# Performance work log

Hardware: AMD Instinct MI355X
Metric: run time of the kernel (lower is better)

Reference implementation:

```python
import jax, jax.numpy as jnp
import numpy as np
from jax import lax

EPS = 1e-5
DN = ('NCHW', 'OIHW', 'NCHW')


def fastsign(x):
    # forward: sign(x); (STE backward handled in fwdbwd module)
    return jnp.sign(x)


def batchnorm(x, gamma, beta, mean, var):
    # inference-mode BatchNorm2d over channel dim
    inv = gamma / jnp.sqrt(var + EPS)
    return x * inv[None, :, None, None] + (beta - mean * inv)[None, :, None, None]


def avgpool2x2(x):
    B, C, H, W = x.shape
    return x.reshape(B, C, H // 2, 2, W // 2, 2).mean(axis=(3, 5))


def setup_inputs() -> dict:
    key = jax.random.key(0)
    ks = jax.random.split(key, 8)
    inp, B, H, W = 256, 32, 56, 56
    x = jax.random.normal(ks[0], (B, inp, H, W), dtype=jnp.float32)
    w3 = jax.random.normal(ks[1], (inp, inp, 3, 3), dtype=jnp.float32) * 0.05
    g3 = jax.random.uniform(ks[2], (inp,), dtype=jnp.float32, minval=0.5, maxval=1.5)
    b3 = jax.random.normal(ks[3], (inp,), dtype=jnp.float32) * 0.1
    m3 = jax.random.normal(ks[4], (inp,), dtype=jnp.float32) * 0.1
    v3 = jax.random.uniform(ks[5], (inp,), dtype=jnp.float32, minval=0.5, maxval=1.5)
    w1 = jax.random.normal(ks[6], (2 * inp, inp, 1, 1), dtype=jnp.float32) * 0.05
    k2 = jax.random.split(ks[7], 4)
    g1 = jax.random.uniform(k2[0], (2 * inp,), dtype=jnp.float32, minval=0.5, maxval=1.5)
    b1 = jax.random.normal(k2[1], (2 * inp,), dtype=jnp.float32) * 0.1
    m1 = jax.random.normal(k2[2], (2 * inp,), dtype=jnp.float32) * 0.1
    v1 = jax.random.uniform(k2[3], (2 * inp,), dtype=jnp.float32, minval=0.5, maxval=1.5)
    return {"x": x, "w3": w3, "g3": g3, "b3": b3, "m3": m3, "v3": v3,
            "w1": w1, "g1": g1, "b1": b1, "m1": m1, "v1": v1}


def reference(x, w3, g3, b3, m3, v3, w1, g1, b1, m1, v1):
    stride = 2
    # --- conv3x3 branch: binarize act + binarize weight, stride-2 3x3 conv, BN ---
    y = lax.conv_general_dilated(fastsign(x), fastsign(w3),
                                 window_strides=(stride, stride),
                                 padding=((1, 1), (1, 1)),
                                 dimension_numbers=DN)
    y = batchnorm(y, g3, b3, m3, v3)
    # shortcut1: AvgPool2d(2,2) when stride==2
    h = y + avgpool2x2(x)
    # --- pointwise branch: 1x1 binary conv doubling channels, BN ---
    z = lax.conv_general_dilated(fastsign(h), fastsign(w1),
                                 window_strides=(1, 1),
                                 padding=((0, 0), (0, 0)),
                                 dimension_numbers=DN)
    z = batchnorm(z, g1, b1, m1, v1)
    # shortcut2: duplicate channels
    return z + jnp.concatenate((h, h), axis=1)
```

## Files before the change

kernel.cpp:

```cpp
#include <hip/hip_runtime.h>
#include <stdint.h>

#define BB   32
#define CC1  256
#define HH   56
#define WW   56
#define PH   57
#define OHH  28
#define OWW  28
#define NPIX (OHH*OWW)
#define CC2  512
#define EPSV 1e-5f

typedef unsigned short ushortx8 __attribute__((ext_vector_type(8)));

static __device__ __forceinline__ int popc64(uint64_t v) {
    return __builtin_popcountll(v);
}
static __device__ __forceinline__ unsigned short f2bf(float f) {
    uint32_t u = __float_as_uint(f);
    u += 0x7FFFu + ((u >> 16) & 1u);
    return (unsigned short)(u >> 16);
}
static __device__ __forceinline__ float bf2f(unsigned short u) {
    return __uint_as_float(((uint32_t)u) << 16);
}

__global__ __launch_bounds__(256) void k_binpool(const float* __restrict__ x,
                                                 uint64_t* __restrict__ xbp,
                                                 uint64_t* __restrict__ hbits,
                                                 unsigned short* __restrict__ pool) {
    int gid = blockIdx.x * 256 + threadIdx.x;
    hbits[gid] = 0ull;
    if (gid < 7296) {
        int b = gid / 228, r = gid % 228;
        xbp[((size_t)(b * PH) * PH + (r >> 2)) * 4 + (r & 3)] = 0ull;
    } else if (gid < 14464) {
        int i = gid - 7296;
        int b = i / 224, r = i % 224;
        xbp[((size_t)(b * PH + (r >> 2) + 1) * PH) * 4 + (r & 3)] = 0ull;
    }

    int cell = gid % NPIX;
    int cg   = (gid / NPIX) & 3;
    int b    = gid / (NPIX * 4);
    int pw = cell % OWW;
    int ph = cell / OWW;
    int h0 = 2 * ph, w0 = 2 * pw;
    const float* base = x + ((size_t)(b * CC1 + cg * 64)) * (HH * WW) + h0 * WW + w0;

    uint64_t s00 = 0, s01 = 0, s10 = 0, s11 = 0;
    for (int j = 0; j < 8; ++j) {
        ushortx8 pv;
        #pragma unroll
        for (int i = 0; i < 8; ++i) {
            int c = j * 8 + i;
            const float* cp = base + (size_t)c * (HH * WW);
            float2 a = *(const float2*)(cp);
            float2 d = *(const float2*)(cp + WW);
            s00 |= (uint64_t)(a.x >= 0.0f) << c;
            s01 |= (uint64_t)(a.y >= 0.0f) << c;
            s10 |= (uint64_t)(d.x >= 0.0f) << c;
            s11 |= (uint64_t)(d.y >= 0.0f) << c;
            pv[i] = f2bf(0.25f * (a.x + a.y + d.x + d.y));
        }
        *(ushortx8*)(pool + ((size_t)((b * 32 + cg * 8 + j) * NPIX + cell)) * 8) = pv;
    }

    size_t rb = ((size_t)(b * PH + h0 + 1) * PH + w0 + 1) * 4 + cg;
    xbp[rb]          = s00;
    xbp[rb + 4]      = s01;
    xbp[rb + PH * 4]     = s10;
    xbp[rb + PH * 4 + 4] = s11;
}

__global__ __launch_bounds__(256) void k_packw3(const float* __restrict__ w3,
                                                uint64_t* __restrict__ w3t) {
    int id = blockIdx.x * 256 + threadIdx.x;
    int k   = id % 4;
    int tap = (id / 4) % 9;
    int oc  = id / 36;
    const float* wp = w3 + (size_t)oc * 2304 + (size_t)(k * 64) * 9 + tap;
    uint64_t bits = 0;
    #pragma unroll 8
    for (int c = 0; c < 64; ++c) {
        bits |= (uint64_t)(wp[c * 9] >= 0.0f) << c;
    }
    w3t[((size_t)tap * CC1 + oc) * 4 + k] = bits;
}

__global__ __launch_bounds__(256) void k_prep2(const float* __restrict__ w1,
                                               uint64_t* __restrict__ w1b,
                                               const uint64_t* __restrict__ w3t,
                                               const float* __restrict__ g3,
                                               const float* __restrict__ b3,
                                               const float* __restrict__ m3,
                                               const float* __restrict__ v3,
                                               const float* __restrict__ g1,
                                               const float* __restrict__ b1,
                                               const float* __restrict__ m1,
                                               const float* __restrict__ v1,
                                               float* __restrict__ sc3,
                                               float* __restrict__ bi3,
                                               float* __restrict__ sc1,
                                               float* __restrict__ bi1,
                                               int* __restrict__ ctop,
                                               int* __restrict__ cleft,
                                               int* __restrict__ ccorn) {
    int id = blockIdx.x * 256 + threadIdx.x;
    int k  = id % 4;
    int oc = id / 4;
    const float* wp = w1 + (size_t)oc * 256 + k * 64;
    uint64_t bits = 0;
    #pragma unroll 8
    for (int c = 0; c < 64; ++c) {
        bits |= (uint64_t)(wp[c] >= 0.0f) << c;
    }
    w1b[(size_t)oc * 4 + k] = bits;
    if (k == 0) {
        float s1 = g1[oc] / sqrtf(v1[oc] + EPSV);
        sc1[oc] = s1;
        bi1[oc] = b1[oc] - m1[oc] * s1;
        if (oc < CC1) {
            float s3 = g3[oc] / sqrtf(v3[oc] + EPSV);
            sc3[oc] = s3;
            bi3[oc] = b3[oc] - m3[oc] * s3;
        }
    }
    if (id < CC1) {
        int pt[9];
        #pragma unroll
        for (int t = 0; t < 9; ++t) {
            const uint64_t* p = w3t + ((size_t)t * CC1 + id) * 4;
            pt[t] = popc64(p[0]) + popc64(p[1]) + popc64(p[2]) + popc64(p[3]);
        }
        ctop[id]  = (256 - 2 * pt[0]) + (256 - 2 * pt[1]) + (256 - 2 * pt[2]);
        cleft[id] = (256 - 2 * pt[0]) + (256 - 2 * pt[3]) + (256 - 2 * pt[6]);
        ccorn[id] = (256 - 2 * pt[0]);
    }
}

__global__ __launch_bounds__(256, 4) void k_conv3(const uint64_t* __restrict__ xbp,
                                                  const uint64_t* __restrict__ w3t,
                                                  const float* __restrict__ sc3,
                                                  const float* __restrict__ bi3,
                                                  const int* __restrict__ ctop,
                                                  const int* __restrict__ cleft,
                                                  const int* __restrict__ ccorn,
                                                  const unsigned short* __restrict__ pool,
                                                  unsigned short* __restrict__ hbuf,
                                                  uint64_t* __restrict__ hbits) {
    int loc = blockIdx.x * 256 + threadIdx.x;
    int p  = loc % NPIX;
    int ow = p % OWW;
    int oh = p / OWW;
    int b  = loc / NPIX;
    int ocg = blockIdx.y;

    int tot[8] = {0, 0, 0, 0, 0, 0, 0, 0};
    for (int kh = 0; kh < 3; ++kh) {
        const uint64_t* rp = xbp + ((size_t)((b * PH + 2 * oh + kh) * PH) + 2 * ow) * 4;
        uint64_t t0[4], t1[4], t2[4];
        #pragma unroll
        for (int k = 0; k < 4; ++k) { t0[k] = rp[k]; t1[k] = rp[4 + k]; t2[k] = rp[8 + k]; }
        const uint64_t* wrow = w3t + ((size_t)(kh * 3) * CC1 + ocg * 8) * 4;
        #pragma unroll
        for (int o = 0; o < 8; ++o) {
            const uint64_t* w0  = wrow + (size_t)o * 4;
            const uint64_t* w1p = w0 + (size_t)CC1 * 4;
            const uint64_t* w2p = w0 + (size_t)CC1 * 8;
            int s = tot[o];
            #pragma unroll
            for (int k = 0; k < 4; ++k) s += popc64(t0[k] ^ w0[k]);
            #pragma unroll
            for (int k = 0; k < 4; ++k) s += popc64(t1[k] ^ w1p[k]);
            #pragma unroll
            for (int k = 0; k < 4; ++k) s += popc64(t2[k] ^ w2p[k]);
            tot[o] = s;
        }
    }

    ushortx8 pv = *(const ushortx8*)(pool + ((size_t)((b * 32 + ocg) * NPIX + p)) * 8);

    bool top  = (oh == 0);
    bool left = (ow == 0);
    uint64_t hb = 0;
    #pragma unroll
    for (int o = 0; o < 8; ++o) {
        int oc = ocg * 8 + o;
        int corr = (top ? ctop[oc] : 0) + (left ? cleft[oc] : 0)
                 - ((top && left) ? ccorn[oc] : 0);
        float y = (float)(2304 - 2 * tot[o] - corr);
        float hv = y * sc3[oc] + bi3[oc] + bf2f(pv[o]);
        hbuf[((size_t)(b * CC1 + oc)) * NPIX + p] = f2bf(hv);
        hb |= (uint64_t)(hv >= 0.0f) << ((ocg & 7) * 8 + o);
    }
    atomicOr((unsigned long long*)&hbits[(size_t)loc * 4 + (ocg >> 3)],
             (unsigned long long)hb);
}

__global__ __launch_bounds__(256, 4) void k_conv1(const uint64_t* __restrict__ hbits,
                                                  const uint64_t* __restrict__ w1b,
                                                  const unsigned short* __restrict__ hbuf,
                                                  const float* __restrict__ sc1,
                                                  const float* __restrict__ bi1,
                                                  float* __restrict__ out) {
    int loc = blockIdx.x * 256 + threadIdx.x;
    int p = loc % NPIX;
    int b = loc / NPIX;
    int ocg = blockIdx.y;

    uint64_t hw[4];
    const uint64_t* hp = hbits + (size_t)loc * 4;
    #pragma unroll
    for (int k = 0; k < 4; ++k) hw[k] = hp[k];

    #pragma unroll
    for (int o = 0; o < 8; ++o) {
        int oc  = ocg * 8 + o;
        int oc2 = oc + CC1;
        const uint64_t* wa = w1b + (size_t)oc  * 4;
        const uint64_t* wb = w1b + (size_t)oc2 * 4;
        int pa = 0, pb = 0;
        #pragma unroll
        for (int k = 0; k < 4; ++k) pa += popc64(hw[k] ^ wa[k]);
        #pragma unroll
        for (int k = 0; k < 4; ++k) pb += popc64(hw[k] ^ wb[k]);
        float hc = bf2f(hbuf[((size_t)(b * CC1 + oc)) * NPIX + p]);
        float za = (float)(256 - 2 * pa) * sc1[oc]  + bi1[oc]  + hc;
        float zb = (float)(256 - 2 * pb) * sc1[oc2] + bi1[oc2] + hc;
        out[((size_t)(b * CC2 + oc))  * NPIX + p] = za;
        out[((size_t)(b * CC2 + oc2)) * NPIX + p] = zb;
    }
}

extern "C" void kernel_launch(void* const* d_in, const int* in_sizes, int n_in,
                              void* d_out, int out_size, void* d_ws, size_t ws_size,
                              hipStream_t stream) {
    const float* x  = (const float*)d_in[0];
    const float* w3 = (const float*)d_in[1];
    const float* g3 = (const float*)d_in[2];
    const float* b3 = (const float*)d_in[3];
    const float* m3 = (const float*)d_in[4];
    const float* v3 = (const float*)d_in[5];
    const float* w1 = (const float*)d_in[6];
    const float* g1 = (const float*)d_in[7];
    const float* b1 = (const float*)d_in[8];
    const float* m1 = (const float*)d_in[9];
    const float* v1 = (const float*)d_in[10];
    float* out = (float*)d_out;

    uint8_t* ws = (uint8_t*)d_ws;
    size_t off = 0;
    uint64_t* xbp   = (uint64_t*)(ws + off); off += (size_t)BB * PH * PH * 4 * 8;
    uint64_t* hbits = (uint64_t*)(ws + off); off += (size_t)BB * NPIX * 4 * 8;
    uint64_t* w3t   = (uint64_t*)(ws + off); off += (size_t)9 * CC1 * 4 * 8;
    uint64_t* w1b   = (uint64_t*)(ws + off); off += (size_t)CC2 * 4 * 8;
    float* sc3 = (float*)(ws + off); off += CC1 * 4;
    float* bi3 = (float*)(ws + off); off += CC1 * 4;
    float* sc1 = (float*)(ws + off); off += CC2 * 4;
    float* bi1 = (float*)(ws + off); off += CC2 * 4;
    int* ctop  = (int*)(ws + off); off += CC1 * 4;
    int* cleft = (int*)(ws + off); off += CC1 * 4;
    int* ccorn = (int*)(ws + off); off += CC1 * 4;
    unsigned short* pool   = (unsigned short*)(ws + off); off += (size_t)BB * CC1 * NPIX * 2;
    unsigned short* hbuf16 = (unsigned short*)(ws + off); off += (size_t)BB * CC1 * NPIX * 2;

    k_binpool<<<dim3(100352 / 256), 256, 0, stream>>>(x, xbp, hbits, pool);
    k_packw3 <<<dim3(9216 / 256),   256, 0, stream>>>(w3, w3t);
    k_prep2  <<<dim3(2048 / 256),   256, 0, stream>>>(w1, w1b, w3t, g3, b3, m3, v3,
                                                      g1, b1, m1, v1, sc3, bi3, sc1, bi1,
                                                      ctop, cleft, ccorn);
    k_conv3  <<<dim3(98, 32), 256, 0, stream>>>(xbp, w3t, sc3, bi3, ctop, cleft, ccorn,
                                                pool, hbuf16, hbits);
    k_conv1  <<<dim3(98, 32), 256, 0, stream>>>(hbits, w1b, hbuf16, sc1, bi1, out);
}
```

Baseline: 90.09 us.

## Fuse binary 3x3 conv and pointwise conv into one kernel via shared sign bits

Merges the stride-2 binary 3x3 conv kernel and the 1x1 binary conv kernel into a single kernel. Each block handles 16 pixels across all 256 channels, with 16 thread groups of 16 channels each, and exchanges the sign bits of h through shared memory. This removes the bf16 h buffer round trip, the hbits zeroing and the atomicOr. The 3x3 weights are relaid out per output channel, so each thread reads 12 contiguous words per kernel row. The cost is more registers per thread (16 accumulators plus 16 h values) and fewer threads per block working on distinct pixels, which may hurt coalescing of the output stores.

```diff
diff --git a/kernel.cpp b/kernel.cpp
--- a/kernel.cpp
+++ b/kernel.cpp
@@ -28,10 +28,8 @@
 
 __global__ __launch_bounds__(256) void k_binpool(const float* __restrict__ x,
                                                  uint64_t* __restrict__ xbp,
-                                                 uint64_t* __restrict__ hbits,
                                                  unsigned short* __restrict__ pool) {
     int gid = blockIdx.x * 256 + threadIdx.x;
-    hbits[gid] = 0ull;
     if (gid < 7296) {
         int b = gid / 228, r = gid % 228;
         xbp[((size_t)(b * PH) * PH + (r >> 2)) * 4 + (r & 3)] = 0ull;
@@ -68,14 +66,14 @@
     }
 
     size_t rb = ((size_t)(b * PH + h0 + 1) * PH + w0 + 1) * 4 + cg;
-    xbp[rb]          = s00;
-    xbp[rb + 4]      = s01;
+    xbp[rb]              = s00;
+    xbp[rb + 4]          = s01;
     xbp[rb + PH * 4]     = s10;
     xbp[rb + PH * 4 + 4] = s11;
 }
 
 __global__ __launch_bounds__(256) void k_packw3(const float* __restrict__ w3,
-                                                uint64_t* __restrict__ w3t) {
+                                                uint64_t* __restrict__ w3o) {
     int id = blockIdx.x * 256 + threadIdx.x;
     int k   = id % 4;
     int tap = (id / 4) % 9;
@@ -86,12 +84,12 @@
     for (int c = 0; c < 64; ++c) {
         bits |= (uint64_t)(wp[c * 9] >= 0.0f) << c;
     }
-    w3t[((size_t)tap * CC1 + oc) * 4 + k] = bits;
+    w3o[(size_t)oc * 36 + tap * 4 + k] = bits;
 }
 
 __global__ __launch_bounds__(256) void k_prep2(const float* __restrict__ w1,
                                                uint64_t* __restrict__ w1b,
-                                               const uint64_t* __restrict__ w3t,
+                                               const uint64_t* __restrict__ w3o,
                                                const float* __restrict__ g3,
                                                const float* __restrict__ b3,
                                                const float* __restrict__ m3,
@@ -131,7 +129,7 @@
         int pt[9];
         #pragma unroll
         for (int t = 0; t < 9; ++t) {
-            const uint64_t* p = w3t + ((size_t)t * CC1 + id) * 4;
+            const uint64_t* p = w3o + (size_t)id * 36 + t * 4;
             pt[t] = popc64(p[0]) + popc64(p[1]) + popc64(p[2]) + popc64(p[3]);
         }
         ctop[id]  = (256 - 2 * pt[0]) + (256 - 2 * pt[1]) + (256 - 2 * pt[2]);
@@ -140,84 +138,76 @@
     }
 }
 
-__global__ __launch_bounds__(256, 4) void k_conv3(const uint64_t* __restrict__ xbp,
-                                                  const uint64_t* __restrict__ w3t,
+__global__ __launch_bounds__(256, 4) void k_fused(const uint64_t* __restrict__ xbp,
+                                                  const uint64_t* __restrict__ w3o,
                                                   const float* __restrict__ sc3,
                                                   const float* __restrict__ bi3,
                                                   const int* __restrict__ ctop,
                                                   const int* __restrict__ cleft,
                                                   const int* __restrict__ ccorn,
                                                   const unsigned short* __restrict__ pool,
-                                                  unsigned short* __restrict__ hbuf,
-                                                  uint64_t* __restrict__ hbits) {
-    int loc = blockIdx.x * 256 + threadIdx.x;
-    int p  = loc % NPIX;
+                                                  const uint64_t* __restrict__ w1b,
+                                                  const float* __restrict__ sc1,
+                                                  const float* __restrict__ bi1,
+                                                  float* __restrict__ out) {
+    __shared__ uint64_t hswq[16][4];
+
+    int tid  = threadIdx.x;
+    int pixl = tid & 15;
+    int g    = tid >> 4;
+    int b    = blockIdx.x / 49;
+    int p    = (blockIdx.x % 49) * 16 + pixl;
     int ow = p % OWW;
     int oh = p / OWW;
-    int b  = loc / NPIX;
-    int ocg = blockIdx.y;
-
-    int tot[8] = {0, 0, 0, 0, 0, 0, 0, 0};
+
+    int tot[16];
+    #pragma unroll
+    for (int o = 0; o < 16; ++o) tot[o] = 0;
+
     for (int kh = 0; kh < 3; ++kh) {
         const uint64_t* rp = xbp + ((size_t)((b * PH + 2 * oh + kh) * PH) + 2 * ow) * 4;
-        uint64_t t0[4], t1[4], t2[4];
-        #pragma unroll
-        for (int k = 0; k < 4; ++k) { t0[k] = rp[k]; t1[k] = rp[4 + k]; t2[k] = rp[8 + k]; }
-        const uint64_t* wrow = w3t + ((size_t)(kh * 3) * CC1 + ocg * 8) * 4;
-        #pragma unroll
-        for (int o = 0; o < 8; ++o) {
-            const uint64_t* w0  = wrow + (size_t)o * 4;
-            const uint64_t* w1p = w0 + (size_t)CC1 * 4;
-            const uint64_t* w2p = w0 + (size_t)CC1 * 8;
+        uint64_t tw[12];
+        #pragma unroll
+        for (int k = 0; k < 12; ++k) tw[k] = rp[k];
+        const uint64_t* wg = w3o + (size_t)(g * 16) * 36 + kh * 12;
+        #pragma unroll
+        for (int o = 0; o < 16; ++o) {
+            const uint64_t* wp = wg + (size_t)o * 36;
             int s = tot[o];
             #pragma unroll
-            for (int k = 0; k < 4; ++k) s += popc64(t0[k] ^ w0[k]);
-            #pragma unroll
-            for (int k = 0; k < 4; ++k) s += popc64(t1[k] ^ w1p[k]);
-            #pragma unroll
-            for (int k = 0; k < 4; ++k) s += popc64(t2[k] ^ w2p[k]);
+            for (int k = 0; k < 12; ++k) s += popc64(tw[k] ^ wp[k]);
             tot[o] = s;
         }
     }
 
-    ushortx8 pv = *(const ushortx8*)(pool + ((size_t)((b * 32 + ocg) * NPIX + p)) * 8);
+    ushortx8 pv0 = *(const ushortx8*)(pool + ((size_t)((b * 32 + g * 2    ) * NPIX + p)) * 8);
+    ushortx8 pv1 = *(const ushortx8*)(pool + ((size_t)((b * 32 + g * 2 + 1) * NPIX + p)) * 8);
 
     bool top  = (oh == 0);
     bool left = (ow == 0);
-    uint64_t hb = 0;
-    #pragma unroll
-    for (int o = 0; o < 8; ++o) {
-        int oc = ocg * 8 + o;
+    float hreg[16];
+    unsigned int hs = 0;
+    #pragma unroll
+    for (int o = 0; o < 16; ++o) {
+        int oc = g * 16 + o;
         int corr = (top ? ctop[oc] : 0) + (left ? cleft[oc] : 0)
                  - ((top && left) ? ccorn[oc] : 0);
         float y = (float)(2304 - 2 * tot[o] - corr);
-        float hv = y * sc3[oc] + bi3[oc] + bf2f(pv[o]);
-        hbuf[((size_t)(b * CC1 + oc)) * NPIX + p] = f2bf(hv);
-        hb |= (uint64_t)(hv >= 0.0f) << ((ocg & 7) * 8 + o);
-    }
-    atomicOr((unsigned long long*)&hbits[(size_t)loc * 4 + (ocg >> 3)],
-             (unsigned long long)hb);
-}
-
-__global__ __launch_bounds__(256, 4) void k_conv1(const uint64_t* __restrict__ hbits,
-                                                  const uint64_t* __restrict__ w1b,
-                                                  const unsigned short* __restrict__ hbuf,
-                                                  const float* __restrict__ sc1,
-                                                  const float* __restrict__ bi1,
-                                                  float* __restrict__ out) {
-    int loc = blockIdx.x * 256 + threadIdx.x;
-    int p = loc % NPIX;
-    int b = loc / NPIX;
-    int ocg = blockIdx.y;
+        float pl = bf2f(o < 8 ? pv0[o & 7] : pv1[o & 7]);
+        float hv = y * sc3[oc] + bi3[oc] + pl;
+        hreg[o] = hv;
+        hs |= (unsigned int)(hv >= 0.0f) << o;
+    }
+    ((unsigned short*)hswq)[pixl * 16 + g] = (unsigned short)hs;
+    __syncthreads();
 
     uint64_t hw[4];
-    const uint64_t* hp = hbits + (size_t)loc * 4;
-    #pragma unroll
-    for (int k = 0; k < 4; ++k) hw[k] = hp[k];
-
-    #pragma unroll
-    for (int o = 0; o < 8; ++o) {
-        int oc  = ocg * 8 + o;
+    #pragma unroll
+    for (int k = 0; k < 4; ++k) hw[k] = hswq[pixl][k];
+
+    #pragma unroll
+    for (int o = 0; o < 16; ++o) {
+        int oc  = g * 16 + o;
         int oc2 = oc + CC1;
         const uint64_t* wa = w1b + (size_t)oc  * 4;
         const uint64_t* wb = w1b + (size_t)oc2 * 4;
@@ -226,11 +216,9 @@
         for (int k = 0; k < 4; ++k) pa += popc64(hw[k] ^ wa[k]);
         #pragma unroll
         for (int k = 0; k < 4; ++k) pb += popc64(hw[k] ^ wb[k]);
-        float hc = bf2f(hbuf[((size_t)(b * CC1 + oc)) * NPIX + p]);
-        float za = (float)(256 - 2 * pa) * sc1[oc]  + bi1[oc]  + hc;
-        float zb = (float)(256 - 2 * pb) * sc1[oc2] + bi1[oc2] + hc;
-        out[((size_t)(b * CC2 + oc))  * NPIX + p] = za;
-        out[((size_t)(b * CC2 + oc2)) * NPIX + p] = zb;
+        float hc = hreg[o];
+        out[((size_t)(b * CC2 + oc))  * NPIX + p] = (float)(256 - 2 * pa) * sc1[oc]  + bi1[oc]  + hc;
+        out[((size_t)(b * CC2 + oc2)) * NPIX + p] = (float)(256 - 2 * pb) * sc1[oc2] + bi1[oc2] + hc;
     }
 }
 
@@ -252,10 +240,9 @@
 
     uint8_t* ws = (uint8_t*)d_ws;
     size_t off = 0;
-    uint64_t* xbp   = (uint64_t*)(ws + off); off += (size_t)BB * PH * PH * 4 * 8;
-    uint64_t* hbits = (uint64_t*)(ws + off); off += (size_t)BB * NPIX * 4 * 8;
-    uint64_t* w3t   = (uint64_t*)(ws + off); off += (size_t)9 * CC1 * 4 * 8;
-    uint64_t* w1b   = (uint64_t*)(ws + off); off += (size_t)CC2 * 4 * 8;
+    uint64_t* xbp = (uint64_t*)(ws + off); off += (size_t)BB * PH * PH * 4 * 8;
+    uint64_t* w3o = (uint64_t*)(ws + off); off += (size_t)CC1 * 36 * 8;
+    uint64_t* w1b = (uint64_t*)(ws + off); off += (size_t)CC2 * 4 * 8;
     float* sc3 = (float*)(ws + off); off += CC1 * 4;
     float* bi3 = (float*)(ws + off); off += CC1 * 4;
     float* sc1 = (float*)(ws + off); off += CC2 * 4;
@@ -263,15 +250,13 @@
     int* ctop  = (int*)(ws + off); off += CC1 * 4;
     int* cleft = (int*)(ws + off); off += CC1 * 4;
     int* ccorn = (int*)(ws + off); off += CC1 * 4;
-    unsigned short* pool   = (unsigned short*)(ws + off); off += (size_t)BB * CC1 * NPIX * 2;
-    unsigned short* hbuf16 = (unsigned short*)(ws + off); off += (size_t)BB * CC1 * NPIX * 2;
-
-    k_binpool<<<dim3(100352 / 256), 256, 0, stream>>>(x, xbp, hbits, pool);
-    k_packw3 <<<dim3(9216 / 256),   256, 0, stream>>>(w3, w3t);
-    k_prep2  <<<dim3(2048 / 256),   256, 0, stream>>>(w1, w1b, w3t, g3, b3, m3, v3,
+    unsigned short* pool = (unsigned short*)(ws + off); off += (size_t)BB * CC1 * NPIX * 2;
+
+    k_binpool<<<dim3(100352 / 256), 256, 0, stream>>>(x, xbp, pool);
+    k_packw3 <<<dim3(9216 / 256),   256, 0, stream>>>(w3, w3o);
+    k_prep2  <<<dim3(2048 / 256),   256, 0, stream>>>(w1, w1b, w3o, g3, b3, m3, v3,
                                                       g1, b1, m1, v1, sc3, bi3, sc1, bi1,
                                                       ctop, cleft, ccorn);
-    k_conv3  <<<dim3(98, 32), 256, 0, stream>>>(xbp, w3t, sc3, bi3, ctop, cleft, ccorn,
-                                                pool, hbuf16, hbits);
-    k_conv1  <<<dim3(98, 32), 256, 0, stream>>>(hbits, w1b, hbuf16, sc1, bi1, out);
-}
+    k_fused  <<<dim3(1568), 256, 0, stream>>>(xbp, w3o, sc3, bi3, ctop, cleft, ccorn,
+                                              pool, w1b, sc1, bi1, out);
+}
```

Measured after the change: 128.1 us. +42.2%, slower.
